# Kernel optimization log

Measured on AMD Instinct MI355X. Metric: run time of the kernel, lower is better.

Reference implementation:

```python
import jax, jax.numpy as jnp
import numpy as np

N = 8192
N_DIM = 7
N_WIDTH = 64


def setup_inputs() -> dict:
    key = jax.random.key(0)
    ks = jax.random.split(key, 12)
    scale = 0.05
    u = lambda k, shape: scale * (2.0 * jax.random.uniform(k, shape) - 1.0)
    # Linear params stored as (in, out) so forward uses x @ W + b (same math as torch Linear).
    lin = lambda k, fan_in, fan_out: (
        jax.random.uniform(jax.random.fold_in(k, 0), (fan_in, fan_out),
                           minval=-1.0, maxval=1.0) / np.sqrt(fan_in),
        jax.random.uniform(jax.random.fold_in(k, 1), (fan_out,),
                           minval=-1.0, maxval=1.0) / np.sqrt(fan_in),
    )
    W1, b1 = lin(ks[1], N_DIM, N_WIDTH)
    W2, b2 = lin(ks[2], N_WIDTH, N_WIDTH)
    Wl, bl = lin(ks[3], N_WIDTH, 1)
    return {
        "x": jax.random.normal(ks[0], (N, N_DIM), dtype=jnp.float32),
        "alpha": jax.random.uniform(ks[4], (1,)),          # Edges.alpha = 1 * rand(1)
        "W1": W1, "b1": b1, "wt1": u(ks[5], (N_WIDTH, N_WIDTH)), "bs1": u(ks[6], (1,)),
        "W2": W2, "b2": b2, "wt2": u(ks[7], (N_WIDTH, N_WIDTH)), "bs2": u(ks[8], (1,)),
        "Wl": Wl, "bl": bl,
    }


def _edges(x, alpha):
    eta, phi = x[:, 1], x[:, 2]
    deta = eta[:, None] - eta[None, :]                      # (n, n)
    dphi = jnp.abs(phi[:, None] - phi[None, :])
    dphi = jnp.where(dphi > jnp.pi, 2.0 * jnp.pi - dphi, dphi)
    dRdR = deta * deta + dphi * dphi
    A = jnp.exp(-alpha[0] * dRdR)
    return jax.nn.softmax(A, axis=1) + jnp.eye(x.shape[0], dtype=x.dtype)


def _gcn_layer(X, A, W, b, wt, bs):
    X = jax.nn.relu(X @ W + b)                              # embed + relu
    X = (A @ X) @ wt + bs[0]                                # aggregate + mix + scalar bias
    return jax.nn.relu(X)


def reference(x, alpha, W1, b1, wt1, bs1, W2, b2, wt2, bs2, Wl, bl):
    A = _edges(x, alpha)
    V = jax.nn.relu(_gcn_layer(x, A, W1, b1, wt1, bs1))
    V = jax.nn.relu(_gcn_layer(V, A, W2, b2, wt2, bs2))
    s = V.sum(axis=0)                                       # (n_width,)
    return jax.nn.sigmoid(s @ Wl + bl)                      # (1,)
```

## Files before the change

### kernel.cpp

```cpp
#include <hip/hip_runtime.h>
#include <hip/hip_bf16.h>
#include <math.h>

#define NN 8192
#define L2E 1.44269504088896340736f
#define TWO_PI 6.28318530717958647693f

typedef _Float16 h8 __attribute__((ext_vector_type(8)));
typedef float f32x4 __attribute__((ext_vector_type(4)));

#define MFMA16(A, B, C) __builtin_amdgcn_mfma_f32_16x16x32_f16(A, B, C, 0, 0, 0)

__global__ __launch_bounds__(256) void prep_kernel(
    const float* __restrict__ x, const float* __restrict__ alpha,
    const float* __restrict__ W1, const float* __restrict__ b1,
    float* __restrict__ eta_s, float* __restrict__ phi,
    float* __restrict__ H1, _Float16* __restrict__ HT1,
    float* __restrict__ svec)
{
  __shared__ float sW[448];
  __shared__ float sb[64];
  __shared__ float T[32][65];
  const int t = threadIdx.x;
  if (blockIdx.x == 0 && t < 64) svec[t] = 0.f;
  for (int k = t; k < 448; k += 256) sW[k] = W1[k];
  if (t < 64) sb[t] = b1[t];
  const float s = sqrtf(alpha[0] * L2E);
  const int i0 = blockIdx.x * 32;
  const int r = t >> 3, q = t & 7;
  const int i = i0 + r;
  float xv[7];
#pragma unroll
  for (int k = 0; k < 7; k++) xv[k] = x[i * 7 + k];
  if (q == 0) { eta_s[i] = xv[1] * s; phi[i] = xv[2]; }
  __syncthreads();
#pragma unroll
  for (int c = 0; c < 8; c++) {
    const int n = q * 8 + c;
    float hv = sb[n];
#pragma unroll
    for (int k = 0; k < 7; k++) hv = fmaf(xv[k], sW[k * 64 + n], hv);
    T[r][n] = fmaxf(hv, 0.f);
  }
  __syncthreads();
  for (int e = t; e < 2048; e += 256) H1[i0 * 64 + e] = T[e >> 6][e & 63];
  const int n = t >> 2, sg = (t & 3) * 8;
  h8 v;
#pragma unroll
  for (int ss = 0; ss < 8; ss++) v[ss] = (_Float16)T[sg + ss][n];
  *(h8*)(HT1 + (size_t)n * NN + i0 + sg) = v;
}

template <bool NEED_L>
__global__ __launch_bounds__(256, 4) void attn_pass(
    const float* __restrict__ eta_s, const float* __restrict__ phi,
    const _Float16* __restrict__ HT, const float* __restrict__ alpha,
    float* __restrict__ Ypart, float* __restrict__ lpart)
{
  const int tid = threadIdx.x;
  const int w = tid >> 6;
  const int lane = tid & 63;
  const int m = lane & 15;
  const int g = lane >> 4;
  const int tile = blockIdx.x >> 2;
  const int part = blockIdx.x & 3;
  const int i0 = tile << 5;
  const float s = sqrtf(alpha[0] * L2E);
  const float et0 = eta_s[i0 + m],      ph0 = phi[i0 + m];
  const float et1 = eta_s[i0 + 16 + m], ph1 = phi[i0 + 16 + m];

  f32x4 a00 = {0,0,0,0}, a01 = {0,0,0,0}, a02 = {0,0,0,0}, a03 = {0,0,0,0};
  f32x4 a10 = {0,0,0,0}, a11 = {0,0,0,0}, a12 = {0,0,0,0}, a13 = {0,0,0,0};
  float l0 = 0.f, l1 = 0.f;

  const int jb = part * 2048 + w * 512 + g * 8;
  const float* ep  = eta_s + jb;
  const float* php = phi + jb;
  const _Float16* h0p = HT + (size_t)(0 * 16 + m) * NN + jb;
  const _Float16* h1p = HT + (size_t)(1 * 16 + m) * NN + jb;
  const _Float16* h2p = HT + (size_t)(2 * 16 + m) * NN + jb;
  const _Float16* h3p = HT + (size_t)(3 * 16 + m) * NN + jb;

  float4 e0 = *(const float4*)ep,  e1 = *(const float4*)(ep + 4);
  float4 p0 = *(const float4*)php, p1 = *(const float4*)(php + 4);
  h8 b0 = *(const h8*)h0p, b1 = *(const h8*)h1p;
  h8 b2 = *(const h8*)h2p, b3 = *(const h8*)h3p;

  for (int it = 0; it < 16; ++it) {
    const float ea[8] = {e0.x, e0.y, e0.z, e0.w, e1.x, e1.y, e1.z, e1.w};
    const float pa[8] = {p0.x, p0.y, p0.z, p0.w, p1.x, p1.y, p1.z, p1.w};
    ep += 32; php += 32;
    e0 = *(const float4*)ep;  e1 = *(const float4*)(ep + 4);
    p0 = *(const float4*)php; p1 = *(const float4*)(php + 4);

    h8 af0, af1;
#pragma unroll
    for (int tt = 0; tt < 8; ++tt) {
      {
        const float dp = ph0 - pa[tt];
        const float wr = fminf(fabsf(dp), TWO_PI - fabsf(dp)) * s;
        const float de = et0 - ea[tt];
        const float r2 = fmaf(de, de, wr * wr);
        const float a  = __builtin_amdgcn_exp2f(-r2);
        const float P  = __builtin_amdgcn_exp2f(fmaf(a, L2E, -L2E));
        if constexpr (NEED_L) l0 += P;
        af0[tt] = (_Float16)P;
      }
      {
        const float dp = ph1 - pa[tt];
        const float wr = fminf(fabsf(dp), TWO_PI - fabsf(dp)) * s;
        const float de = et1 - ea[tt];
        const float r2 = fmaf(de, de, wr * wr);
        const float a  = __builtin_amdgcn_exp2f(-r2);
        const float P  = __builtin_amdgcn_exp2f(fmaf(a, L2E, -L2E));
        if constexpr (NEED_L) l1 += P;
        af1[tt] = (_Float16)P;
      }
    }
    a00 = MFMA16(af0, b0, a00); a01 = MFMA16(af0, b1, a01);
    a02 = MFMA16(af0, b2, a02); a03 = MFMA16(af0, b3, a03);
    a10 = MFMA16(af1, b0, a10); a11 = MFMA16(af1, b1, a11);
    a12 = MFMA16(af1, b2, a12); a13 = MFMA16(af1, b3, a13);
    h0p += 32; h1p += 32; h2p += 32; h3p += 32;
    b0 = *(const h8*)h0p; b1 = *(const h8*)h1p;
    b2 = *(const h8*)h2p; b3 = *(const h8*)h3p;
  }

  __shared__ float red[2][32][66];
  __shared__ float lred2[2][4][32];
  const int h = w >> 1;
  if ((w & 1) == 0) {
#pragma unroll
    for (int r = 0; r < 4; ++r) {
      red[h][g * 4 + r][m]      = a00[r]; red[h][g * 4 + r][16 + m] = a01[r];
      red[h][g * 4 + r][32 + m] = a02[r]; red[h][g * 4 + r][48 + m] = a03[r];
      red[h][16 + g * 4 + r][m]      = a10[r]; red[h][16 + g * 4 + r][16 + m] = a11[r];
      red[h][16 + g * 4 + r][32 + m] = a12[r]; red[h][16 + g * 4 + r][48 + m] = a13[r];
    }
    if constexpr (NEED_L) { lred2[h][g][m] = l0; lred2[h][g][16 + m] = l1; }
  }
  __syncthreads();
  if (w & 1) {
#pragma unroll
    for (int r = 0; r < 4; ++r) {
      red[h][g * 4 + r][m]      += a00[r]; red[h][g * 4 + r][16 + m] += a01[r];
      red[h][g * 4 + r][32 + m] += a02[r]; red[h][g * 4 + r][48 + m] += a03[r];
      red[h][16 + g * 4 + r][m]      += a10[r]; red[h][16 + g * 4 + r][16 + m] += a11[r];
      red[h][16 + g * 4 + r][32 + m] += a12[r]; red[h][16 + g * 4 + r][48 + m] += a13[r];
    }
    if constexpr (NEED_L) { lred2[h][g][m] += l0; lred2[h][g][16 + m] += l1; }
  }
  __syncthreads();
  const int pbase = part * 2;
#pragma unroll
  for (int hh = 0; hh < 2; ++hh) {
#pragma unroll
    for (int k = 0; k < 8; ++k) {
      const int e = tid + k * 256;
      Ypart[((size_t)(pbase + hh) * NN + i0 + (e >> 6)) * 64 + (e & 63)] =
          red[hh][e >> 6][e & 63];
    }
  }
  if constexpr (NEED_L) {
    if (tid < 64) {
      const int hh = tid >> 5, row = tid & 31;
      lpart[(size_t)(pbase + hh) * NN + i0 + row] =
          lred2[hh][0][row] + lred2[hh][1][row] +
          lred2[hh][2][row] + lred2[hh][3][row];
    }
  }
}

__global__ __launch_bounds__(256) void mid_kernel(
    const float* __restrict__ Yp, const float* __restrict__ lp,
    const float* __restrict__ H1, const float* __restrict__ wt1,
    const float* __restrict__ bs1, const float* __restrict__ W2,
    const float* __restrict__ b2, float* __restrict__ H2,
    _Float16* __restrict__ HT2)
{
  __shared__ float sA[64][64];
  __shared__ float sB[64][64];
  __shared__ float U[32][65];
  __shared__ float sb2v[64];
  const int t = threadIdx.x;
  for (int e = t; e < 4096; e += 256) {
    sA[e >> 6][e & 63] = wt1[e];
    sB[e >> 6][e & 63] = W2[e];
  }
  if (t < 64) sb2v[t] = b2[t];
  const float bsv = bs1[0];
  const int i0 = blockIdx.x * 32;
  const int r = t >> 3, q = t & 7;
  const int i = i0 + r;
  float l = 0.f;
#pragma unroll
  for (int p = 0; p < 8; ++p) l += lp[(size_t)p * NN + i];
  const float rl = 1.0f / l;
  f32x4 ya = {0,0,0,0}, yb = {0,0,0,0};
#pragma unroll
  for (int p = 0; p < 8; ++p) {
    ya += *(const f32x4*)(Yp + ((size_t)p * NN + i) * 64 + q * 8);
    yb += *(const f32x4*)(Yp + ((size_t)p * NN + i) * 64 + q * 8 + 4);
  }
  const f32x4 h1a = *(const f32x4*)(H1 + (size_t)i * 64 + q * 8);
  const f32x4 h1b = *(const f32x4*)(H1 + (size_t)i * 64 + q * 8 + 4);
#pragma unroll
  for (int c = 0; c < 4; ++c) {
    U[r][q * 8 + c]     = fmaf(ya[c], rl, h1a[c]);
    U[r][q * 8 + 4 + c] = fmaf(yb[c], rl, h1b[c]);
  }
  __syncthreads();
  float z[8];
#pragma unroll
  for (int c = 0; c < 8; ++c) z[c] = bsv;
  for (int k = 0; k < 64; ++k) {
    const float uk = U[r][k];
#pragma unroll
    for (int c = 0; c < 8; ++c) z[c] = fmaf(uk, sA[k][q * 8 + c], z[c]);
  }
  __syncthreads();
#pragma unroll
  for (int c = 0; c < 8; ++c) U[r][q * 8 + c] = fmaxf(z[c], 0.f);
  __syncthreads();
  float hv[8];
#pragma unroll
  for (int c = 0; c < 8; ++c) hv[c] = sb2v[q * 8 + c];
  for (int k = 0; k < 64; ++k) {
    const float uk = U[r][k];
#pragma unroll
    for (int c = 0; c < 8; ++c) hv[c] = fmaf(uk, sB[k][q * 8 + c], hv[c]);
  }
  __syncthreads();
#pragma unroll
  for (int c = 0; c < 8; ++c) U[r][q * 8 + c] = fmaxf(hv[c], 0.f);
  __syncthreads();
  for (int e = t; e < 2048; e += 256) H2[i0 * 64 + e] = U[e >> 6][e & 63];
  const int n = t >> 2, sg = (t & 3) * 8;
  h8 v;
#pragma unroll
  for (int ss = 0; ss < 8; ss++) v[ss] = (_Float16)U[sg + ss][n];
  *(h8*)(HT2 + (size_t)n * NN + i0 + sg) = v;
}

__global__ __launch_bounds__(256) void final_kernel(
    const float* __restrict__ Yp, const float* __restrict__ lp,
    const float* __restrict__ H2, const float* __restrict__ wt2,
    const float* __restrict__ bs2, float* __restrict__ svec)
{
  __shared__ float sA[64][64];
  __shared__ float U[32][65];
  __shared__ float cred[4][64];
  const int t = threadIdx.x;
  for (int e = t; e < 4096; e += 256) sA[e >> 6][e & 63] = wt2[e];
  const float bsv = bs2[0];
  const int i0 = blockIdx.x * 32;
  const int r = t >> 3, q = t & 7;
  const int i = i0 + r;
  float l = 0.f;
#pragma unroll
  for (int p = 0; p < 8; ++p) l += lp[(size_t)p * NN + i];
  const float rl = 1.0f / l;
  f32x4 ya = {0,0,0,0}, yb = {0,0,0,0};
#pragma unroll
  for (int p = 0; p < 8; ++p) {
    ya += *(const f32x4*)(Yp + ((size_t)p * NN + i) * 64 + q * 8);
    yb += *(const f32x4*)(Yp + ((size_t)p * NN + i) * 64 + q * 8 + 4);
  }
  const f32x4 h2a = *(const f32x4*)(H2 + (size_t)i * 64 + q * 8);
  const f32x4 h2b = *(const f32x4*)(H2 + (size_t)i * 64 + q * 8 + 4);
#pragma unroll
  for (int c = 0; c < 4; ++c) {
    U[r][q * 8 + c]     = fmaf(ya[c], rl, h2a[c]);
    U[r][q * 8 + 4 + c] = fmaf(yb[c], rl, h2b[c]);
  }
  __syncthreads();
  float z[8];
#pragma unroll
  for (int c = 0; c < 8; ++c) z[c] = bsv;
  for (int k = 0; k < 64; ++k) {
    const float uk = U[r][k];
#pragma unroll
    for (int c = 0; c < 8; ++c) z[c] = fmaf(uk, sA[k][q * 8 + c], z[c]);
  }
  __syncthreads();
#pragma unroll
  for (int c = 0; c < 8; ++c) U[r][q * 8 + c] = fmaxf(z[c], 0.f);
  __syncthreads();
  const int col = t & 63, rg = t >> 6;
  float ps = 0.f;
#pragma unroll
  for (int rr = 0; rr < 8; rr++) ps += U[rg * 8 + rr][col];
  cred[rg][col] = ps;
  __syncthreads();
  if (t < 64)
    atomicAdd(svec + t, cred[0][t] + cred[1][t] + cred[2][t] + cred[3][t]);
}

__global__ void out_kernel(const float* __restrict__ svec,
                           const float* __restrict__ Wl,
                           const float* __restrict__ bl,
                           float* __restrict__ out)
{
  const int t = threadIdx.x;
  float v = svec[t] * Wl[t];
#pragma unroll
  for (int off = 32; off > 0; off >>= 1) v += __shfl_down(v, off);
  if (t == 0) {
    const float logit = v + bl[0];
    out[0] = 1.0f / (1.0f + __builtin_amdgcn_exp2f(-logit * L2E));
  }
}

extern "C" void kernel_launch(void* const* d_in, const int* in_sizes, int n_in,
                              void* d_out, int out_size, void* d_ws,
                              size_t ws_size, hipStream_t stream)
{
  const float* x     = (const float*)d_in[0];
  const float* alpha = (const float*)d_in[1];
  const float* W1    = (const float*)d_in[2];
  const float* b1    = (const float*)d_in[3];
  const float* wt1   = (const float*)d_in[4];
  const float* bs1   = (const float*)d_in[5];
  const float* W2    = (const float*)d_in[6];
  const float* b2    = (const float*)d_in[7];
  const float* wt2   = (const float*)d_in[8];
  const float* bs2   = (const float*)d_in[9];
  const float* Wl    = (const float*)d_in[10];
  const float* bl    = (const float*)d_in[11];
  float* out = (float*)d_out;

  char* ws = (char*)d_ws;
  size_t off = 0;
  auto alloc = [&](size_t bytes) {
    void* p = ws + off;
    off = (off + bytes + 255) & ~(size_t)255;
    return p;
  };
  float* eta_s = (float*)alloc(NN * 4 + 256);
  float* phi   = (float*)alloc(NN * 4 + 256);
  float* H1    = (float*)alloc((size_t)NN * 64 * 4);
  float* H2    = (float*)alloc((size_t)NN * 64 * 4);
  float* Ypart = (float*)alloc((size_t)8 * NN * 64 * 4);
  float* lpart = (float*)alloc((size_t)8 * NN * 4);
  _Float16* HT = (_Float16*)alloc((size_t)NN * 64 * 2 + 512);
  float* svec  = (float*)alloc(64 * 4);

  prep_kernel<<<256, 256, 0, stream>>>(x, alpha, W1, b1, eta_s, phi, H1, HT, svec);
  attn_pass<true><<<1024, 256, 0, stream>>>(eta_s, phi, HT, alpha, Ypart, lpart);
  mid_kernel<<<256, 256, 0, stream>>>(Ypart, lpart, H1, wt1, bs1, W2, b2, H2, HT);
  attn_pass<false><<<1024, 256, 0, stream>>>(eta_s, phi, HT, alpha, Ypart, nullptr);
  final_kernel<<<256, 256, 0, stream>>>(Ypart, lpart, H2, wt2, bs2, svec);
  out_kernel<<<1, 64, 0, stream>>>(svec, Wl, bl, out);
}
```

Measured before the change: 192.0 us.

## Split attention into more column parts, pre-scale phi, pack fp16 converts, shrink dense tiles

```diff
diff --git a/kernel.cpp b/kernel.cpp
--- a/kernel.cpp
+++ b/kernel.cpp
@@ -7,6 +7,7 @@
 #define TWO_PI 6.28318530717958647693f
 
 typedef _Float16 h8 __attribute__((ext_vector_type(8)));
+typedef _Float16 h4 __attribute__((ext_vector_type(4)));
 typedef float f32x4 __attribute__((ext_vector_type(4)));
 
 #define MFMA16(A, B, C) __builtin_amdgcn_mfma_f32_16x16x32_f16(A, B, C, 0, 0, 0)
@@ -14,7 +15,7 @@
 __global__ __launch_bounds__(256) void prep_kernel(
     const float* __restrict__ x, const float* __restrict__ alpha,
     const float* __restrict__ W1, const float* __restrict__ b1,
-    float* __restrict__ eta_s, float* __restrict__ phi,
+    float* __restrict__ eta_s, float* __restrict__ phi_s,
     float* __restrict__ H1, _Float16* __restrict__ HT1,
     float* __restrict__ svec)
 {
@@ -32,7 +33,7 @@
   float xv[7];
 #pragma unroll
   for (int k = 0; k < 7; k++) xv[k] = x[i * 7 + k];
-  if (q == 0) { eta_s[i] = xv[1] * s; phi[i] = xv[2]; }
+  if (q == 0) { eta_s[i] = xv[1] * s; phi_s[i] = xv[2] * s; }
   __syncthreads();
 #pragma unroll
   for (int c = 0; c < 8; c++) {
@@ -52,8 +53,8 @@
 }
 
 template <bool NEED_L>
-__global__ __launch_bounds__(256, 4) void attn_pass(
-    const float* __restrict__ eta_s, const float* __restrict__ phi,
+__global__ __launch_bounds__(256, 6) void attn_pass(
+    const float* __restrict__ eta_s, const float* __restrict__ phi_s,
     const _Float16* __restrict__ HT, const float* __restrict__ alpha,
     float* __restrict__ Ypart, float* __restrict__ lpart)
 {
@@ -62,20 +63,20 @@
   const int lane = tid & 63;
   const int m = lane & 15;
   const int g = lane >> 4;
-  const int tile = blockIdx.x >> 2;
-  const int part = blockIdx.x & 3;
+  const int tile = blockIdx.x >> 3;
+  const int part = blockIdx.x & 7;
   const int i0 = tile << 5;
-  const float s = sqrtf(alpha[0] * L2E);
-  const float et0 = eta_s[i0 + m],      ph0 = phi[i0 + m];
-  const float et1 = eta_s[i0 + 16 + m], ph1 = phi[i0 + 16 + m];
+  const float Cs = TWO_PI * sqrtf(alpha[0] * L2E);
+  const float et0 = eta_s[i0 + m],      ph0 = phi_s[i0 + m];
+  const float et1 = eta_s[i0 + 16 + m], ph1 = phi_s[i0 + 16 + m];
 
   f32x4 a00 = {0,0,0,0}, a01 = {0,0,0,0}, a02 = {0,0,0,0}, a03 = {0,0,0,0};
   f32x4 a10 = {0,0,0,0}, a11 = {0,0,0,0}, a12 = {0,0,0,0}, a13 = {0,0,0,0};
   float l0 = 0.f, l1 = 0.f;
 
-  const int jb = part * 2048 + w * 512 + g * 8;
+  const int jb = part * 1024 + w * 256 + g * 8;
   const float* ep  = eta_s + jb;
-  const float* php = phi + jb;
+  const float* php = phi_s + jb;
   const _Float16* h0p = HT + (size_t)(0 * 16 + m) * NN + jb;
   const _Float16* h1p = HT + (size_t)(1 * 16 + m) * NN + jb;
   const _Float16* h2p = HT + (size_t)(2 * 16 + m) * NN + jb;
@@ -86,41 +87,49 @@
   h8 b0 = *(const h8*)h0p, b1 = *(const h8*)h1p;
   h8 b2 = *(const h8*)h2p, b3 = *(const h8*)h3p;
 
-  for (int it = 0; it < 16; ++it) {
+  union AF { h8 v; decltype(__builtin_amdgcn_cvt_pkrtz(0.f, 0.f)) p[4]; };
+
+  for (int it = 0; it < 8; ++it) {
     const float ea[8] = {e0.x, e0.y, e0.z, e0.w, e1.x, e1.y, e1.z, e1.w};
     const float pa[8] = {p0.x, p0.y, p0.z, p0.w, p1.x, p1.y, p1.z, p1.w};
     ep += 32; php += 32;
     e0 = *(const float4*)ep;  e1 = *(const float4*)(ep + 4);
     p0 = *(const float4*)php; p1 = *(const float4*)(php + 4);
 
-    h8 af0, af1;
-#pragma unroll
-    for (int tt = 0; tt < 8; ++tt) {
-      {
-        const float dp = ph0 - pa[tt];
-        const float wr = fminf(fabsf(dp), TWO_PI - fabsf(dp)) * s;
-        const float de = et0 - ea[tt];
-        const float r2 = fmaf(de, de, wr * wr);
-        const float a  = __builtin_amdgcn_exp2f(-r2);
-        const float P  = __builtin_amdgcn_exp2f(fmaf(a, L2E, -L2E));
-        if constexpr (NEED_L) l0 += P;
-        af0[tt] = (_Float16)P;
+    AF af0, af1;
+#pragma unroll
+    for (int tt = 0; tt < 8; tt += 2) {
+      float P[4];
+#pragma unroll
+      for (int u = 0; u < 2; ++u) {
+        {
+          const float dp = ph0 - pa[tt + u];
+          const float wr = fminf(fabsf(dp), Cs - fabsf(dp));
+          const float de = et0 - ea[tt + u];
+          const float r2 = fmaf(de, de, wr * wr);
+          const float a  = __builtin_amdgcn_exp2f(-r2);
+          const float pv = __builtin_amdgcn_exp2f(fmaf(a, L2E, -L2E));
+          if constexpr (NEED_L) l0 += pv;
+          P[u] = pv;
+        }
+        {
+          const float dp = ph1 - pa[tt + u];
+          const float wr = fminf(fabsf(dp), Cs - fabsf(dp));
+          const float de = et1 - ea[tt + u];
+          const float r2 = fmaf(de, de, wr * wr);
+          const float a  = __builtin_amdgcn_exp2f(-r2);
+          const float pv = __builtin_amdgcn_exp2f(fmaf(a, L2E, -L2E));
+          if constexpr (NEED_L) l1 += pv;
+          P[2 + u] = pv;
+        }
       }
-      {
-        const float dp = ph1 - pa[tt];
-        const float wr = fminf(fabsf(dp), TWO_PI - fabsf(dp)) * s;
-        const float de = et1 - ea[tt];
-        const float r2 = fmaf(de, de, wr * wr);
-        const float a  = __builtin_amdgcn_exp2f(-r2);
-        const float P  = __builtin_amdgcn_exp2f(fmaf(a, L2E, -L2E));
-        if constexpr (NEED_L) l1 += P;
-        af1[tt] = (_Float16)P;
-      }
+      af0.p[tt >> 1] = __builtin_amdgcn_cvt_pkrtz(P[0], P[1]);
+      af1.p[tt >> 1] = __builtin_amdgcn_cvt_pkrtz(P[2], P[3]);
     }
-    a00 = MFMA16(af0, b0, a00); a01 = MFMA16(af0, b1, a01);
-    a02 = MFMA16(af0, b2, a02); a03 = MFMA16(af0, b3, a03);
-    a10 = MFMA16(af1, b0, a10); a11 = MFMA16(af1, b1, a11);
-    a12 = MFMA16(af1, b2, a12); a13 = MFMA16(af1, b3, a13);
+    a00 = MFMA16(af0.v, b0, a00); a01 = MFMA16(af0.v, b1, a01);
+    a02 = MFMA16(af0.v, b2, a02); a03 = MFMA16(af0.v, b3, a03);
+    a10 = MFMA16(af1.v, b0, a10); a11 = MFMA16(af1.v, b1, a11);
+    a12 = MFMA16(af1.v, b2, a12); a13 = MFMA16(af1.v, b3, a13);
     h0p += 32; h1p += 32; h2p += 32; h3p += 32;
     b0 = *(const h8*)h0p; b1 = *(const h8*)h1p;
     b2 = *(const h8*)h2p; b3 = *(const h8*)h3p;
@@ -151,22 +160,20 @@
     if constexpr (NEED_L) { lred2[h][g][m] += l0; lred2[h][g][16 + m] += l1; }
   }
   __syncthreads();
-  const int pbase = part * 2;
-#pragma unroll
-  for (int hh = 0; hh < 2; ++hh) {
-#pragma unroll
-    for (int k = 0; k < 8; ++k) {
-      const int e = tid + k * 256;
-      Ypart[((size_t)(pbase + hh) * NN + i0 + (e >> 6)) * 64 + (e & 63)] =
-          red[hh][e >> 6][e & 63];
-    }
+#pragma unroll
+  for (int k = 0; k < 8; ++k) {
+    const int e = tid + k * 256;
+    Ypart[((size_t)part * NN + i0 + (e >> 6)) * 64 + (e & 63)] =
+        red[0][e >> 6][e & 63] + red[1][e >> 6][e & 63];
   }
   if constexpr (NEED_L) {
-    if (tid < 64) {
-      const int hh = tid >> 5, row = tid & 31;
-      lpart[(size_t)(pbase + hh) * NN + i0 + row] =
-          lred2[hh][0][row] + lred2[hh][1][row] +
-          lred2[hh][2][row] + lred2[hh][3][row];
+    if (tid < 32) {
+      float s = 0.f;
+#pragma unroll
+      for (int hh = 0; hh < 2; ++hh)
+#pragma unroll
+        for (int gg = 0; gg < 4; ++gg) s += lred2[hh][gg][tid];
+      lpart[(size_t)part * NN + i0 + tid] = s;
     }
   }
 }
@@ -178,9 +185,9 @@
     const float* __restrict__ b2, float* __restrict__ H2,
     _Float16* __restrict__ HT2)
 {
-  __shared__ float sA[64][64];
-  __shared__ float sB[64][64];
-  __shared__ float U[32][65];
+  __shared__ float sA[64][68];
+  __shared__ float sB[64][68];
+  __shared__ float U[16][65];
   __shared__ float sb2v[64];
   const int t = threadIdx.x;
   for (int e = t; e < 4096; e += 256) {
@@ -189,57 +196,53 @@
   }
   if (t < 64) sb2v[t] = b2[t];
   const float bsv = bs1[0];
-  const int i0 = blockIdx.x * 32;
-  const int r = t >> 3, q = t & 7;
+  const int i0 = blockIdx.x * 16;
+  const int r = t >> 4, q = t & 15;
   const int i = i0 + r;
   float l = 0.f;
 #pragma unroll
   for (int p = 0; p < 8; ++p) l += lp[(size_t)p * NN + i];
   const float rl = 1.0f / l;
-  f32x4 ya = {0,0,0,0}, yb = {0,0,0,0};
-#pragma unroll
-  for (int p = 0; p < 8; ++p) {
-    ya += *(const f32x4*)(Yp + ((size_t)p * NN + i) * 64 + q * 8);
-    yb += *(const f32x4*)(Yp + ((size_t)p * NN + i) * 64 + q * 8 + 4);
-  }
-  const f32x4 h1a = *(const f32x4*)(H1 + (size_t)i * 64 + q * 8);
-  const f32x4 h1b = *(const f32x4*)(H1 + (size_t)i * 64 + q * 8 + 4);
-#pragma unroll
-  for (int c = 0; c < 4; ++c) {
-    U[r][q * 8 + c]     = fmaf(ya[c], rl, h1a[c]);
-    U[r][q * 8 + 4 + c] = fmaf(yb[c], rl, h1b[c]);
-  }
-  __syncthreads();
-  float z[8];
-#pragma unroll
-  for (int c = 0; c < 8; ++c) z[c] = bsv;
+  f32x4 ya = {0, 0, 0, 0};
+#pragma unroll
+  for (int p = 0; p < 8; ++p)
+    ya += *(const f32x4*)(Yp + ((size_t)p * NN + i) * 64 + q * 4);
+  const f32x4 h1 = *(const f32x4*)(H1 + (size_t)i * 64 + q * 4);
+#pragma unroll
+  for (int c = 0; c < 4; ++c) U[r][q * 4 + c] = fmaf(ya[c], rl, h1[c]);
+  __syncthreads();
+  float z[4];
+#pragma unroll
+  for (int c = 0; c < 4; ++c) z[c] = bsv;
   for (int k = 0; k < 64; ++k) {
     const float uk = U[r][k];
-#pragma unroll
-    for (int c = 0; c < 8; ++c) z[c] = fmaf(uk, sA[k][q * 8 + c], z[c]);
-  }
-  __syncthreads();
-#pragma unroll
-  for (int c = 0; c < 8; ++c) U[r][q * 8 + c] = fmaxf(z[c], 0.f);
-  __syncthreads();
-  float hv[8];
-#pragma unroll
-  for (int c = 0; c < 8; ++c) hv[c] = sb2v[q * 8 + c];
+    const f32x4 sa = *(const f32x4*)&sA[k][q * 4];
+#pragma unroll
+    for (int c = 0; c < 4; ++c) z[c] = fmaf(uk, sa[c], z[c]);
+  }
+  __syncthreads();
+#pragma unroll
+  for (int c = 0; c < 4; ++c) U[r][q * 4 + c] = fmaxf(z[c], 0.f);
+  __syncthreads();
+  float hv[4];
+#pragma unroll
+  for (int c = 0; c < 4; ++c) hv[c] = sb2v[q * 4 + c];
   for (int k = 0; k < 64; ++k) {
     const float uk = U[r][k];
-#pragma unroll
-    for (int c = 0; c < 8; ++c) hv[c] = fmaf(uk, sB[k][q * 8 + c], hv[c]);
-  }
-  __syncthreads();
-#pragma unroll
-  for (int c = 0; c < 8; ++c) U[r][q * 8 + c] = fmaxf(hv[c], 0.f);
-  __syncthreads();
-  for (int e = t; e < 2048; e += 256) H2[i0 * 64 + e] = U[e >> 6][e & 63];
-  const int n = t >> 2, sg = (t & 3) * 8;
-  h8 v;
-#pragma unroll
-  for (int ss = 0; ss < 8; ss++) v[ss] = (_Float16)U[sg + ss][n];
-  *(h8*)(HT2 + (size_t)n * NN + i0 + sg) = v;
+    const f32x4 sb4 = *(const f32x4*)&sB[k][q * 4];
+#pragma unroll
+    for (int c = 0; c < 4; ++c) hv[c] = fmaf(uk, sb4[c], hv[c]);
+  }
+  __syncthreads();
+#pragma unroll
+  for (int c = 0; c < 4; ++c) U[r][q * 4 + c] = fmaxf(hv[c], 0.f);
+  __syncthreads();
+  for (int e = t; e < 1024; e += 256) H2[i0 * 64 + e] = U[e >> 6][e & 63];
+  const int n = t >> 2, sg = (t & 3) * 4;
+  h4 v;
+#pragma unroll
+  for (int ss = 0; ss < 4; ss++) v[ss] = (_Float16)U[sg + ss][n];
+  *(h4*)(HT2 + (size_t)n * NN + i0 + sg) = v;
 }
 
 __global__ __launch_bounds__(256) void final_kernel(
@@ -247,49 +250,44 @@
     const float* __restrict__ H2, const float* __restrict__ wt2,
     const float* __restrict__ bs2, float* __restrict__ svec)
 {
-  __shared__ float sA[64][64];
-  __shared__ float U[32][65];
+  __shared__ float sA[64][68];
+  __shared__ float U[16][65];
   __shared__ float cred[4][64];
   const int t = threadIdx.x;
   for (int e = t; e < 4096; e += 256) sA[e >> 6][e & 63] = wt2[e];
   const float bsv = bs2[0];
-  const int i0 = blockIdx.x * 32;
-  const int r = t >> 3, q = t & 7;
+  const int i0 = blockIdx.x * 16;
+  const int r = t >> 4, q = t & 15;
   const int i = i0 + r;
   float l = 0.f;
 #pragma unroll
   for (int p = 0; p < 8; ++p) l += lp[(size_t)p * NN + i];
   const float rl = 1.0f / l;
-  f32x4 ya = {0,0,0,0}, yb = {0,0,0,0};
-#pragma unroll
-  for (int p = 0; p < 8; ++p) {
-    ya += *(const f32x4*)(Yp + ((size_t)p * NN + i) * 64 + q * 8);
-    yb += *(const f32x4*)(Yp + ((size_t)p * NN + i) * 64 + q * 8 + 4);
-  }
-  const f32x4 h2a = *(const f32x4*)(H2 + (size_t)i * 64 + q * 8);
-  const f32x4 h2b = *(const f32x4*)(H2 + (size_t)i * 64 + q * 8 + 4);
-#pragma unroll
-  for (int c = 0; c < 4; ++c) {
-    U[r][q * 8 + c]     = fmaf(ya[c], rl, h2a[c]);
-    U[r][q * 8 + 4 + c] = fmaf(yb[c], rl, h2b[c]);
-  }
-  __syncthreads();
-  float z[8];
-#pragma unroll
-  for (int c = 0; c < 8; ++c) z[c] = bsv;
+  f32x4 ya = {0, 0, 0, 0};
+#pragma unroll
+  for (int p = 0; p < 8; ++p)
+    ya += *(const f32x4*)(Yp + ((size_t)p * NN + i) * 64 + q * 4);
+  const f32x4 h2 = *(const f32x4*)(H2 + (size_t)i * 64 + q * 4);
+#pragma unroll
+  for (int c = 0; c < 4; ++c) U[r][q * 4 + c] = fmaf(ya[c], rl, h2[c]);
+  __syncthreads();
+  float z[4];
+#pragma unroll
+  for (int c = 0; c < 4; ++c) z[c] = bsv;
   for (int k = 0; k < 64; ++k) {
     const float uk = U[r][k];
-#pragma unroll
-    for (int c = 0; c < 8; ++c) z[c] = fmaf(uk, sA[k][q * 8 + c], z[c]);
-  }
-  __syncthreads();
-#pragma unroll
-  for (int c = 0; c < 8; ++c) U[r][q * 8 + c] = fmaxf(z[c], 0.f);
+    const f32x4 sa = *(const f32x4*)&sA[k][q * 4];
+#pragma unroll
+    for (int c = 0; c < 4; ++c) z[c] = fmaf(uk, sa[c], z[c]);
+  }
+  __syncthreads();
+#pragma unroll
+  for (int c = 0; c < 4; ++c) U[r][q * 4 + c] = fmaxf(z[c], 0.f);
   __syncthreads();
   const int col = t & 63, rg = t >> 6;
   float ps = 0.f;
 #pragma unroll
-  for (int rr = 0; rr < 8; rr++) ps += U[rg * 8 + rr][col];
+  for (int rr = 0; rr < 4; rr++) ps += U[rg * 4 + rr][col];
   cred[rg][col] = ps;
   __syncthreads();
   if (t < 64)
@@ -337,7 +335,7 @@
     return p;
   };
   float* eta_s = (float*)alloc(NN * 4 + 256);
-  float* phi   = (float*)alloc(NN * 4 + 256);
+  float* phi_s = (float*)alloc(NN * 4 + 256);
   float* H1    = (float*)alloc((size_t)NN * 64 * 4);
   float* H2    = (float*)alloc((size_t)NN * 64 * 4);
   float* Ypart = (float*)alloc((size_t)8 * NN * 64 * 4);
@@ -345,10 +343,10 @@
   _Float16* HT = (_Float16*)alloc((size_t)NN * 64 * 2 + 512);
   float* svec  = (float*)alloc(64 * 4);
 
-  prep_kernel<<<256, 256, 0, stream>>>(x, alpha, W1, b1, eta_s, phi, H1, HT, svec);
-  attn_pass<true><<<1024, 256, 0, stream>>>(eta_s, phi, HT, alpha, Ypart, lpart);
-  mid_kernel<<<256, 256, 0, stream>>>(Ypart, lpart, H1, wt1, bs1, W2, b2, H2, HT);
-  attn_pass<false><<<1024, 256, 0, stream>>>(eta_s, phi, HT, alpha, Ypart, nullptr);
-  final_kernel<<<256, 256, 0, stream>>>(Ypart, lpart, H2, wt2, bs2, svec);
+  prep_kernel<<<256, 256, 0, stream>>>(x, alpha, W1, b1, eta_s, phi_s, H1, HT, svec);
+  attn_pass<true><<<2048, 256, 0, stream>>>(eta_s, phi_s, HT, alpha, Ypart, lpart);
+  mid_kernel<<<512, 256, 0, stream>>>(Ypart, lpart, H1, wt1, bs1, W2, b2, H2, HT);
+  attn_pass<false><<<2048, 256, 0, stream>>>(eta_s, phi_s, HT, alpha, Ypart, nullptr);
+  final_kernel<<<512, 256, 0, stream>>>(Ypart, lpart, H2, wt2, bs2, svec);
   out_kernel<<<1, 64, 0, stream>>>(svec, Wl, bl, out);
 }
```

After: 230.9 us. 1.2x slower.
